# Optimization experiments

Hardware: AMD Instinct MI355X
Metric: run time of the kernel (lower is better)

The kernel has to match this reference:

```python
import jax, jax.numpy as jnp
import numpy as np
from jax import lax

MASK_ID = 0  # sequence_mask pad token

def setup_inputs() -> dict:
    key = jax.random.key(0)
    ks = jax.random.split(key, 7)
    B, T, V, E, U_, O = 256, 128, 10000, 256, 1024, 1024
    return {
        "sequences": jax.random.randint(ks[0], (B, T), 0, V),
        "emb_table": jax.random.normal(ks[1], (V, E), jnp.float32) * 0.02,
        "W": jax.random.normal(ks[2], (E, 4 * U_), jnp.float32) * (1.0 / np.sqrt(E)),
        "U": jax.random.normal(ks[3], (U_, 4 * U_), jnp.float32) * (1.0 / np.sqrt(U_)),
        "b": jnp.zeros((4 * U_,), jnp.float32),
        "fc_W": jax.random.normal(ks[4], (U_, O), jnp.float32) * (1.0 / np.sqrt(U_)),
        "fc_b": jnp.zeros((O,), jnp.float32),
    }

def reference(sequences, emb_table, W, U, b, fc_W, fc_b):
    B, T = sequences.shape
    units = U.shape[0]
    # sequence_length_fn: count of non-pad tokens per row
    lengths = jnp.sum(sequences != MASK_ID, axis=1)  # [B]
    x = emb_table[sequences]                          # [B,T,E]
    # precompute input-to-gate contribution (fuses gate matmuls across time)
    x_gates = jnp.einsum('bte,eg->btg', x, W) + b     # [B,T,4U]
    valid = (jnp.arange(T)[:, None] < lengths[None, :])  # [T,B]

    def step(carry, inp):
        h, c = carry
        xg, v = inp                                   # [B,4U], [B]
        z = xg + h @ U
        i, f, g, o = jnp.split(z, 4, axis=-1)         # keras gate order i,f,c,o
        i = jax.nn.sigmoid(i)
        f = jax.nn.sigmoid(f)
        o = jax.nn.sigmoid(o)
        g = jnp.tanh(g)
        c_new = f * c + i * g
        h_new = o * jnp.tanh(c_new)
        vm = v[:, None]
        # dynamic_rnn: zero output past length, carry state through
        h_out = jnp.where(vm, h_new, 0.0)
        return (jnp.where(vm, h_new, h), jnp.where(vm, c_new, c)), h_out

    init = (jnp.zeros((B, units), x.dtype), jnp.zeros((B, units), x.dtype))
    _, outs = lax.scan(step, init, (jnp.swapaxes(x_gates, 0, 1), valid))
    outputs = jnp.swapaxes(outs, 0, 1)                # [B,T,U]
    return outputs @ fc_W + fc_b                      # [B,T,O]
```

## Files before the change

kernel.cpp:

```cpp
#include <hip/hip_runtime.h>

typedef short bf16x8 __attribute__((ext_vector_type(8)));
typedef float f32x4  __attribute__((ext_vector_type(4)));
typedef int   i32x4  __attribute__((ext_vector_type(4)));

#define DEVINL __device__ __forceinline__

static constexpr size_t SZ_WIM  = 4096ull * 512 * 2;
static constexpr size_t SZ_FCW  = 1024ull * 2048 * 2;
static constexpr size_t SZ_UIM  = 8388608;
static constexpr size_t SZ_EBI  = 10000ull * 512 * 2;
static constexpr size_t SZ_HH   = 33ull * 524288;
static constexpr size_t SZ_CB   = 1048576;
static constexpr size_t SZ_LEN  = 4096;
static constexpr size_t SZ_DIAG = 2048;

DEVINL unsigned short bf16rn(float x){
  unsigned u = __float_as_uint(x);
  unsigned r = (u + 0x7fffu + ((u >> 16) & 1u)) >> 16;
  return (unsigned short)r;
}
DEVINL unsigned short bf16lo(float x){
  unsigned ub = __float_as_uint(x);
  return bf16rn(x - __uint_as_float(ub & 0xffff0000u));
}
DEVINL float sigm(float x){ return 1.f / (1.f + __expf(-x)); }
DEVINL float tanhfast(float x){
  float xc = fminf(15.f, fmaxf(-15.f, x));
  float e = __expf(2.f * xc);
  return (e - 1.f) / (e + 1.f);
}
DEVINL void gl_lds16(const void* g, void* l){
  __builtin_amdgcn_global_load_lds(
      (const __attribute__((address_space(1))) unsigned*)g,
      (__attribute__((address_space(3))) unsigned*)l, 16, 0, 0);
}
DEVINL int hslot(int t){ return t % 33; }

__global__ void __launch_bounds__(256) probe_fill(float* __restrict__ out, int n, float v)
{
  int i = blockIdx.x * 256 + threadIdx.x;
  if (i < n) out[i] = (i == 0) ? v : 0.f;
}

__global__ void __launch_bounds__(64) diag_check(const int* __restrict__ prog,
                                                 float* __restrict__ out)
{
  if (threadIdx.x == 0){
    int miss = 0;
    for (int i = 7; i >= 1; i--) if (prog[i] == 0) miss = i;
    if (miss){
      for (int k = 0; k < 1024; k++) out[k] = 100.0f + (float)miss;
    }
  }
}

__global__ void __launch_bounds__(128) len_kernel(const int* __restrict__ seq,
                                                  int* __restrict__ len,
                                                  int* __restrict__ prog)
{
  int b = blockIdx.x, t = threadIdx.x;
  if (b == 0 && t == 0) prog[1] = 1;
  int pred = (seq[b * 128 + t] != 0) ? 1 : 0;
  unsigned long long m = __ballot(pred);
  __shared__ int cnt[2];
  if ((t & 63) == 0) cnt[t >> 6] = __popcll(m);
  __syncthreads();
  if (t == 0) len[b] = cnt[0] + cnt[1];
}

__global__ void __launch_bounds__(256) prep_split_img(
    const float* __restrict__ S, unsigned short* __restrict__ img, int N, int Ksrc,
    int* __restrict__ prog, int stage)
{
  __shared__ float tile[64][65];
  const int nt = N >> 6;
  const int bn = blockIdx.x % nt, bk = blockIdx.x / nt;
  const int tid = threadIdx.x;
  if (blockIdx.x == 0 && tid == 0) prog[stage] = 1;
  {
    const int kk = tid >> 6, n = tid & 63;
#pragma unroll 4
    for (int i = 0; i < 16; i++){
      int k = i * 4 + kk;
      tile[k][n] = S[(size_t)((bk << 6) + k) * N + (bn << 6) + n];
    }
  }
  __syncthreads();
  {
    const int n4 = tid >> 6, k = tid & 63;
#pragma unroll 4
    for (int i = 0; i < 16; i++){
      int n = i * 4 + n4;
      float v = tile[k][n];
      size_t rowoff = (size_t)((bn << 6) + n) * (2 * Ksrc) + (bk << 6) + k;
      img[rowoff] = (unsigned short)(__float_as_uint(v) >> 16);
      img[rowoff + Ksrc] = bf16lo(v);
    }
  }
}

__global__ void __launch_bounds__(256) prep_emb_img(const float* __restrict__ emb,
                                                    unsigned short* __restrict__ img)
{
  const int v = blockIdx.x, t = threadIdx.x;
  float x = emb[(size_t)v * 256 + t];
  img[(size_t)v * 512 + t]       = (unsigned short)(__float_as_uint(x) >> 16);
  img[(size_t)v * 512 + 256 + t] = bf16lo(x);
}

__global__ void __launch_bounds__(256) prep_uimg(const float* __restrict__ U,
                                                 signed char* __restrict__ img,
                                                 int* __restrict__ prog)
{
  const int bid = blockIdx.x;
  const int nb = bid >> 2, nt4 = bid & 3;
  const int tid = threadIdx.x;
  if (bid == 0 && tid == 0) prog[4] = 1;
  __shared__ signed char lc[16384], ldq[16384];
  const int colbase = nt4 * 1024 + (nb << 4);
  const int kk = tid >> 4, cc = tid & 15;
#pragma unroll 4
  for (int it = 0; it < 64; it++){
    int k = it * 16 + kk;
    float v = U[(size_t)k * 4096 + colbase + cc];
    int q = (int)rintf(v * 131072.f);
    q = q > 32639 ? 32639 : (q < -32639 ? -32639 : q);
    int a = (q + 128) >> 8;
    int d = q - (a << 8);
    lc[(k << 4) + cc]  = (signed char)a;
    ldq[(k << 4) + cc] = (signed char)d;
  }
  __syncthreads();
#pragma unroll
  for (int rep = 0; rep < 4; rep++){
    int idx = rep * 256 + tid;
    int kt = idx >> 6, lane = idx & 63;
    int n = lane & 15, quad = lane >> 4;
    union { signed char b[16]; i32x4 v; } cb_, db_;
#pragma unroll
    for (int j = 0; j < 16; j++){
      int k = (kt << 6) + (quad << 4) + j;
      cb_.b[j] = lc[(k << 4) + n];
      db_.b[j] = ldq[(k << 4) + n];
    }
    size_t base = (size_t)((((nb << 2) + nt4) * 16 + kt) * 2) * 1024;
    *(i32x4*)(img + base + (size_t)lane * 16)        = cb_.v;
    *(i32x4*)(img + base + 1024 + (size_t)lane * 16) = db_.v;
  }
}

__global__ void __launch_bounds__(256) gemm_gates(
    const unsigned short* __restrict__ Aimg, const unsigned short* __restrict__ Bimg,
    const float* __restrict__ bias, unsigned short* __restrict__ D,
    const int* __restrict__ seq, int c0, int tcsh, int* __restrict__ prog)
{
  __shared__ __align__(16) char lds[32768];
  __shared__ int stok[128];
  const int tid = threadIdx.x, lane = tid & 63, wv = tid >> 6;
  const int quad = lane >> 4, nlo = lane & 15;
  const int wm = wv & 1, wn = wv >> 1;
  const int rowbase = (blockIdx.x >> 5) << 7;
  const int colbase = (blockIdx.x & 31) << 7;
  const int tcm1 = (1 << tcsh) - 1;
  if (blockIdx.x == 0 && tid == 0) prog[5] = 1;
  if (tid < 128){
    int r = rowbase + tid;
    stok[tid] = seq[((r >> tcsh) << 7) + c0 + (r & tcm1)];
  }
  __syncthreads();

  f32x4 acc[4][4];
#pragma unroll
  for (int i = 0; i < 4; i++)
#pragma unroll
    for (int j = 0; j < 4; j++) acc[i][j] = (f32x4){0.f, 0.f, 0.f, 0.f};

  const unsigned short* asrc[2]; const unsigned short* bsrc[2];
  char* adst[2]; char* bdst[2];
#pragma unroll
  for (int p = 0; p < 2; p++){
    int gidx = p * 256 + tid;
    int row = gidx >> 2, sg = gidx & 3;
    int sgs = sg ^ ((row >> 1) & 3);
    asrc[p] = Aimg + (size_t)stok[row] * 512 + sgs * 8;
    bsrc[p] = Bimg + (size_t)(colbase + row) * 512 + sgs * 8;
    adst[p] = &lds[p * 4096 + wv * 1024];
    bdst[p] = &lds[16384 + p * 4096 + wv * 1024];
  }

  auto stage = [&](int c, int cur){
    int k0 = c * 32;
    int seg = (k0 >= 512) ? 2 : (k0 >= 256 ? 1 : 0);
    int acol = k0 - seg * 256;
    int aoff = (seg == 1 ? 256 : 0) + acol;
    int boff = (seg == 2 ? 256 : 0) + acol;
#pragma unroll
    for (int p = 0; p < 2; p++){
      gl_lds16(asrc[p] + aoff, adst[p] + cur * 8192);
      gl_lds16(bsrc[p] + boff, bdst[p] + cur * 8192);
    }
  };

  stage(0, 0);
  int cur = 0;
#pragma unroll 2
  for (int c = 0; c < 24; c++){
    __syncthreads();
    if (c + 1 < 24) stage(c + 1, cur ^ 1);
    bf16x8 af[4], bfr[4];
#pragma unroll
    for (int mt = 0; mt < 4; mt++){
      int r = wm * 64 + mt * 16 + nlo;
      af[mt] = *(const bf16x8*)(&lds[cur * 8192 + r * 64 + ((quad ^ ((r >> 1) & 3)) << 4)]);
    }
#pragma unroll
    for (int nt = 0; nt < 4; nt++){
      int r = wn * 64 + nt * 16 + nlo;
      bfr[nt] = *(const bf16x8*)(&lds[16384 + cur * 8192 + r * 64 + ((quad ^ ((r >> 1) & 3)) << 4)]);
    }
#pragma unroll
    for (int mt = 0; mt < 4; mt++)
#pragma unroll
      for (int nt = 0; nt < 4; nt++)
        acc[mt][nt] = __builtin_amdgcn_mfma_f32_16x16x32_bf16(af[mt], bfr[nt], acc[mt][nt], 0, 0, 0);
    cur ^= 1;
  }

  float bs[4];
#pragma unroll
  for (int nt = 0; nt < 4; nt++) bs[nt] = bias[colbase + wn * 64 + nt * 16 + nlo];
#pragma unroll
  for (int mt = 0; mt < 4; mt++)
#pragma unroll
    for (int nt = 0; nt < 4; nt++){
      int col = colbase + wn * 64 + nt * 16 + nlo;
#pragma unroll
      for (int r = 0; r < 4; r++){
        int row = rowbase + wm * 64 + mt * 16 + quad * 4 + r;
        float v = acc[mt][nt][r] + bs[nt];
        int q = (int)rintf(v * 16384.f);
        q = q > 32767 ? 32767 : (q < -32767 ? -32767 : q);
        D[(size_t)row * 4096 + col] = (unsigned short)(short)q;
      }
    }
}

__global__ void __launch_bounds__(256) gemm_out(
    const unsigned short* __restrict__ ohol, const unsigned short* __restrict__ Bimg,
    const float* __restrict__ bias, float* __restrict__ D,
    int c0, int tcsh, int* __restrict__ prog)
{
  __shared__ __align__(16) char lds[32768];
  const int tid = threadIdx.x, lane = tid & 63, wv = tid >> 6;
  const int quad = lane >> 4, nlo = lane & 15;
  const int wm = wv & 1, wn = wv >> 1;
  const int rowbase = (blockIdx.x >> 3) << 7;
  const int colbase = (blockIdx.x & 7) << 7;
  const int tcm1 = (1 << tcsh) - 1;
  if (blockIdx.x == 0 && tid == 0) prog[7] = 1;

  f32x4 acc[4][4];
#pragma unroll
  for (int i = 0; i < 4; i++)
#pragma unroll
    for (int j = 0; j < 4; j++) acc[i][j] = (f32x4){0.f, 0.f, 0.f, 0.f};

  const unsigned short* asrc[2]; const unsigned short* bsrc[2];
  char* adst[2]; char* bdst[2];
#pragma unroll
  for (int p = 0; p < 2; p++){
    int gidx = p * 256 + tid;
    int row = gidx >> 2, sg = gidx & 3;
    int sgs = sg ^ ((row >> 1) & 3);
    asrc[p] = ohol + (size_t)(rowbase + row) * 2048 + sgs * 8;
    bsrc[p] = Bimg + (size_t)(colbase + row) * 2048 + sgs * 8;
    adst[p] = &lds[p * 4096 + wv * 1024];
    bdst[p] = &lds[16384 + p * 4096 + wv * 1024];
  }

  auto stage = [&](int c, int cur){
    int k0 = c * 32;
    int seg = (k0 >= 2048) ? 2 : (k0 >= 1024 ? 1 : 0);
    int acol = k0 - seg * 1024;
    int aoff = (seg == 1 ? 1024 : 0) + acol;
    int boff = (seg == 2 ? 1024 : 0) + acol;
#pragma unroll
    for (int p = 0; p < 2; p++){
      gl_lds16(asrc[p] + aoff, adst[p] + cur * 8192);
      gl_lds16(bsrc[p] + boff, bdst[p] + cur * 8192);
    }
  };

  stage(0, 0);
  int cur = 0;
#pragma unroll 2
  for (int c = 0; c < 96; c++){
    __syncthreads();
    if (c + 1 < 96) stage(c + 1, cur ^ 1);
    bf16x8 af[4], bfr[4];
#pragma unroll
    for (int mt = 0; mt < 4; mt++){
      int r = wm * 64 + mt * 16 + nlo;
      af[mt] = *(const bf16x8*)(&lds[cur * 8192 + r * 64 + ((quad ^ ((r >> 1) & 3)) << 4)]);
    }
#pragma unroll
    for (int nt = 0; nt < 4; nt++){
      int r = wn * 64 + nt * 16 + nlo;
      bfr[nt] = *(const bf16x8*)(&lds[16384 + cur * 8192 + r * 64 + ((quad ^ ((r >> 1) & 3)) << 4)]);
    }
#pragma unroll
    for (int mt = 0; mt < 4; mt++)
#pragma unroll
      for (int nt = 0; nt < 4; nt++)
        acc[mt][nt] = __builtin_amdgcn_mfma_f32_16x16x32_bf16(af[mt], bfr[nt], acc[mt][nt], 0, 0, 0);
    cur ^= 1;
  }

  float bs[4];
#pragma unroll
  for (int nt = 0; nt < 4; nt++) bs[nt] = bias[colbase + wn * 64 + nt * 16 + nlo];
#pragma unroll
  for (int mt = 0; mt < 4; mt++)
#pragma unroll
    for (int nt = 0; nt < 4; nt++){
      int col = colbase + wn * 64 + nt * 16 + nlo;
#pragma unroll
      for (int r = 0; r < 4; r++){
        int row = rowbase + wm * 64 + mt * 16 + quad * 4 + r;
        int drow = ((row >> tcsh) << 7) + c0 + (row & tcm1);
        D[(size_t)drow * 1024 + col] = acc[mt][nt][r] + bs[nt];
      }
    }
}

DEVINL void mbbar(int* flags, int nb, int t, int wv, int lane){
  __syncthreads();
  if (wv == 0){
    if (lane == 0)
      __hip_atomic_store(&flags[nb], t + 1, __ATOMIC_RELAXED, __HIP_MEMORY_SCOPE_AGENT);
    const int tgt = t + 1;
    for (;;){
      int v = __hip_atomic_load(&flags[lane], __ATOMIC_RELAXED, __HIP_MEMORY_SCOPE_AGENT);
      if (__ballot(v >= tgt) == ~0ull) break;
      __builtin_amdgcn_s_sleep(1);
    }
    __builtin_amdgcn_fence(__ATOMIC_ACQUIRE, "workgroup");
  }
  __syncthreads();
}

__global__ void __launch_bounds__(512, 2) lstm_rec(
    const unsigned short* __restrict__ xq,
    const signed char* __restrict__ uimg,
    const int* __restrict__ len,
    signed char* __restrict__ hh,
    float* __restrict__ cbuf,
    unsigned short* __restrict__ ohol,
    int* __restrict__ barbase,
    int* __restrict__ prog,
    int c0, int tcsh)
{
  __shared__ __align__(16) char lds[50176];
  const int tc = 1 << tcsh;
  const int wg = blockIdx.x, mb = wg >> 6, nb = wg & 63;
  const int tid = threadIdx.x, lane = tid & 63, wv = tid >> 6;
  const int quad = lane >> 4, nlo = lane & 15;
  const int mh = wv & 1, g = wv >> 1;
  int* flags = barbase + (mb << 6);
  if (wg == 0 && tid == 0) prog[6] = 1;

  const unsigned short* hh2 = (const unsigned short*)hh;

  i32x4 Bf[16][2];
#pragma unroll
  for (int kt = 0; kt < 16; kt++)
#pragma unroll
    for (int pl = 0; pl < 2; pl++){
      size_t off = (size_t)((((nb << 2) + g) * 16 + kt) * 2 + pl);
      off = (off * 64 + lane) << 4;
      Bf[kt][pl] = *(const i32x4*)(uimg + off);
    }

  const int erow = tid >> 3;
  const int ecp  = tid & 7;
  const int ecol0 = ecp << 1;
  const int ucol0 = (nb << 4) + ecol0;
  const int bglob = (mb << 6) + erow;
  const int lenr = len[bglob];
  float cst[2], hst[2];
#pragma unroll
  for (int r = 0; r < 2; r++){
    cst[r] = cbuf[(size_t)bglob * 1024 + ucol0 + r];
    unsigned short e = hh2[(size_t)hslot(c0) * 262144 + (size_t)bglob * 1024 + ucol0 + r];
    int a = (signed char)(e >> 8), b_ = (signed char)(e & 255);
    hst[r] = (float)(a * 256 + b_) * (1.0f / 32512.0f);
  }

  const int xrow = tid >> 3, xgt = (tid & 7) >> 1, xhf = tid & 1;
  int4 xreg;
  auto load_x = [&](int s){
    size_t grow = (size_t)((((mb << 6) + xrow) << tcsh) + s);
    xreg = *(const int4*)(xq + grow * 4096 + (xgt << 10) + (nb << 4) + (xhf << 3));
  };
  load_x(0);

  const int hrw = tid >> 3, hsub = tid & 7;

#pragma unroll 1
  for (int s = 0; s < tc; s++){
    const int t = c0 + s;
    const signed char* hsrc = hh + (size_t)hslot(t) * 524288 + (size_t)(mb << 6) * 2048;

    i32x4 accH[2], accM[2], accL[2];
#pragma unroll
    for (int m = 0; m < 2; m++){
      accH[m] = (i32x4){0,0,0,0};
      accM[m] = (i32x4){0,0,0,0};
      accL[m] = (i32x4){0,0,0,0};
    }

    int4 hregA[2], hregB[2];
    auto load_hto = [&](int c, int4* dst){
      const signed char* p = hsrc + (size_t)hrw * 2048 + c * 256 + hsub * 32;
      dst[0] = *(const int4*)p;
      dst[1] = *(const int4*)(p + 16);
    };
    auto write_hf = [&](const int4* src){
      unsigned r0 = (unsigned)src[0].x, r1 = (unsigned)src[0].y;
      unsigned r2 = (unsigned)src[0].z, r3 = (unsigned)src[0].w;
      unsigned r4 = (unsigned)src[1].x, r5 = (unsigned)src[1].y;
      unsigned r6 = (unsigned)src[1].z, r7 = (unsigned)src[1].w;
      i32x4 lo, hi;
      lo[0] = __builtin_amdgcn_perm(r1, r0, 0x06040200u);
      lo[1] = __builtin_amdgcn_perm(r3, r2, 0x06040200u);
      lo[2] = __builtin_amdgcn_perm(r5, r4, 0x06040200u);
      lo[3] = __builtin_amdgcn_perm(r7, r6, 0x06040200u);
      hi[0] = __builtin_amdgcn_perm(r1, r0, 0x07050301u);
      hi[1] = __builtin_amdgcn_perm(r3, r2, 0x07050301u);
      hi[2] = __builtin_amdgcn_perm(r5, r4, 0x07050301u);
      hi[3] = __builtin_amdgcn_perm(r7, r6, 0x07050301u);
      int sw = (hsub ^ (hrw & 7)) << 4;
      *(i32x4*)(&lds[hrw * 128 + sw])        = hi;
      *(i32x4*)(&lds[8192 + hrw * 128 + sw]) = lo;
    };

    load_hto(0, hregA);
    load_hto(1, hregB);

#pragma unroll
    for (int c = 0; c < 8; c++){
      __syncthreads();
      if ((c & 1) == 0) write_hf(hregA); else write_hf(hregB);
      if (c == 0){
        union { int4 v; unsigned short u[8]; } xu; xu.v = xreg;
        const float xs = 1.0f / 16384.f;
        float4 f0, f1;
        f0.x = (float)(short)xu.u[0] * xs; f0.y = (float)(short)xu.u[1] * xs;
        f0.z = (float)(short)xu.u[2] * xs; f0.w = (float)(short)xu.u[3] * xs;
        f1.x = (float)(short)xu.u[4] * xs; f1.y = (float)(short)xu.u[5] * xs;
        f1.z = (float)(short)xu.u[6] * xs; f1.w = (float)(short)xu.u[7] * xs;
        char* xb = &lds[16384 + xrow * 256 + (((xgt << 4) + (xhf << 3)) << 2)];
        *(float4*)xb = f0;
        *(float4*)(xb + 16) = f1;
      }
      __syncthreads();
      if (c + 2 < 8){
        if ((c & 1) == 0) load_hto(c + 2, hregA); else load_hto(c + 2, hregB);
      }
#pragma unroll
      for (int kt2 = 0; kt2 < 2; kt2++){
        const int kt = c * 2 + kt2;
        i32x4 Af[2][2];
#pragma unroll
        for (int m = 0; m < 2; m++){
          int hrow = (mh << 5) + (m << 4) + nlo;
          int sgl = ((kt2 << 2) + quad) ^ (hrow & 7);
          Af[m][0] = *(const i32x4*)(&lds[hrow * 128 + (sgl << 4)]);
          Af[m][1] = *(const i32x4*)(&lds[8192 + hrow * 128 + (sgl << 4)]);
        }
#pragma unroll
        for (int m = 0; m < 2; m++){
          accH[m] = __builtin_amdgcn_mfma_i32_16x16x64_i8(Af[m][0], Bf[kt][0], accH[m], 0, 0, 0);
          accM[m] = __builtin_amdgcn_mfma_i32_16x16x64_i8(Af[m][0], Bf[kt][1], accM[m], 0, 0, 0);
          accM[m] = __builtin_amdgcn_mfma_i32_16x16x64_i8(Af[m][1], Bf[kt][0], accM[m], 0, 0, 0);
          accL[m] = __builtin_amdgcn_mfma_i32_16x16x64_i8(Af[m][1], Bf[kt][1], accL[m], 0, 0, 0);
        }
      }
    }
    __syncthreads();

    if (s + 1 < tc) load_x(s + 1);

    const float cH = 1.0f / 65024.0f;
    const float cM = 1.0f / 16646144.0f;
    const float cL = 1.0f / 4261412864.0f;
#pragma unroll
    for (int m = 0; m < 2; m++){
#pragma unroll
      for (int r = 0; r < 4; r++){
        float z = (float)accH[m][r] * cH
                + (float)accM[m][r] * cM
                + (float)accL[m][r] * cL;
        int zrow = (mh << 5) + (m << 4) + (quad << 2) + r;
        *(float*)(&lds[32768 + (((zrow * 68) + g * 16 + nlo) << 2)]) = z;
      }
    }
    __syncthreads();

    {
      float ho16[2];
      unsigned enc2 = 0;
#pragma unroll
      for (int r = 0; r < 2; r++){
        int col = ecol0 + r;
        float zi = *(const float*)(&lds[32768 + (((erow * 68) + 0  + col) << 2)])
                 + *(const float*)(&lds[16384 + (((erow << 6) + 0  + col) << 2)]);
        float zf = *(const float*)(&lds[32768 + (((erow * 68) + 16 + col) << 2)])
                 + *(const float*)(&lds[16384 + (((erow << 6) + 16 + col) << 2)]);
        float zg = *(const float*)(&lds[32768 + (((erow * 68) + 32 + col) << 2)])
                 + *(const float*)(&lds[16384 + (((erow << 6) + 32 + col) << 2)]);
        float zo = *(const float*)(&lds[32768 + (((erow * 68) + 48 + col) << 2)])
                 + *(const float*)(&lds[16384 + (((erow << 6) + 48 + col) << 2)]);
        float iv = sigm(zi), fv = sigm(zf), ov = sigm(zo), gv = tanhfast(zg);
        float cn = fv * cst[r] + iv * gv;
        float hn = ov * tanhfast(cn);
        bool vld = (t < lenr);
        cst[r] = vld ? cn : cst[r];
        hst[r] = vld ? hn : hst[r];
        ho16[r] = vld ? hn : 0.f;
        int H = (int)rintf(hst[r] * 32512.f);
        H = H > 32512 ? 32512 : (H < -32512 ? -32512 : H);
        int a = (H + 128) >> 8;
        int b_ = H - (a << 8);
        unsigned e = (((unsigned)a & 255u) << 8) | ((unsigned)b_ & 255u);
        enc2 |= e << (r * 16);
      }
      size_t orow = ((size_t)bglob << tcsh) + s;
      unsigned hi2 = (unsigned)(__float_as_uint(ho16[0]) >> 16)
                   | ((unsigned)(__float_as_uint(ho16[1]) >> 16) << 16);
      unsigned lo2 = (unsigned)bf16lo(ho16[0]) | ((unsigned)bf16lo(ho16[1]) << 16);
      *(unsigned*)(ohol + orow * 2048 + ucol0)        = hi2;
      *(unsigned*)(ohol + orow * 2048 + 1024 + ucol0) = lo2;
      unsigned* hp = (unsigned*)(hh + (size_t)hslot(t + 1) * 524288
                                 + ((size_t)bglob * 1024 + ucol0) * 2);
      unsigned old = __hip_atomic_exchange(hp, enc2, __ATOMIC_RELAXED,
                                           __HIP_MEMORY_SCOPE_AGENT);
      asm volatile("" :: "v"(old));
    }
    mbbar(flags, nb, t, wv, lane);
  }

#pragma unroll
  for (int r = 0; r < 2; r++)
    cbuf[(size_t)bglob * 1024 + ucol0 + r] = cst[r];
}

extern "C" void kernel_launch(void* const* d_in, const int* in_sizes, int n_in,
                              void* d_out, int out_size, void* d_ws, size_t ws_size,
                              hipStream_t stream)
{
  const int*   seq = (const int*)  d_in[0];
  const float* emb = (const float*)d_in[1];
  const float* Wm  = (const float*)d_in[2];
  const float* Um  = (const float*)d_in[3];
  const float* bv  = (const float*)d_in[4];
  const float* fcW = (const float*)d_in[5];
  const float* fcb = (const float*)d_in[6];
  float* out = (float*)d_out;
  char* ws = (char*)d_ws;

  hipMemsetAsync(d_out, 0x42, 256, stream);

  size_t off = 0;
  unsigned short* wim = (unsigned short*)(ws + off); off += SZ_WIM;
  unsigned short* fcw = (unsigned short*)(ws + off); off += SZ_FCW;
  signed char*    uim = (signed char*)(ws + off);    off += SZ_UIM;
  unsigned short* ebi = (unsigned short*)(ws + off); off += SZ_EBI;
  signed char*    hh  = (signed char*)(ws + off);    off += SZ_HH;
  float*          cb  = (float*)(ws + off);          off += SZ_CB;
  int*            len = (int*)(ws + off);            off += SZ_LEN;
  int*            diag= (int*)(ws + off);            off += SZ_DIAG;
  const size_t fixed = off;

  int tcsh = -1;
  for (int s = 5; s >= 0; s--)
    if (ws && fixed + (3145728ull << s) <= ws_size){ tcsh = s; break; }

  if (tcsh < 0){
    probe_fill<<<(out_size + 255) / 256, 256, 0, stream>>>(
        out, out_size, 1000.0f + (float)(ws_size >> 20));
    return;
  }
  const int tc = 1 << tcsh;

  unsigned short* xqc  = (unsigned short*)(ws + fixed);
  unsigned short* ohol = (unsigned short*)(ws + fixed + (size_t)tc * 2097152);

  hipMemsetAsync(diag, 0, SZ_DIAG, stream);
  hipMemsetAsync(hh, 0, 524288, stream);
  hipMemsetAsync(cb, 0, SZ_CB, stream);

  int* prog = diag;
  int* barbase = diag + 64;

  len_kernel<<<256, 128, 0, stream>>>(seq, len, prog);
  prep_split_img<<<256, 256, 0, stream>>>(Wm, wim, 4096, 256, prog, 2);
  prep_split_img<<<256, 256, 0, stream>>>(fcW, fcw, 1024, 1024, prog, 3);
  prep_emb_img<<<10000, 256, 0, stream>>>(emb, ebi);
  prep_uimg<<<256, 256, 0, stream>>>(Um, uim, prog);

  for (int c0 = 0; c0 < 128; c0 += tc){
    gemm_gates<<<dim3((2 * tc) * 32), 256, 0, stream>>>(ebi, wim, bv, xqc, seq, c0, tcsh, prog);
    lstm_rec<<<dim3(256), 512, 0, stream>>>(xqc, uim, len, hh, cb, ohol, barbase, prog, c0, tcsh);
    gemm_out<<<dim3((2 * tc) * 8), 256, 0, stream>>>(ohol, fcw, fcb, out, c0, tcsh, prog);
  }

  diag_check<<<1, 64, 0, stream>>>(prog, out);
}
```

Before: 1.880 ms.

## Split recurrent LSTM batch tile across twice as many workgroups

The persistent recurrent kernel now launches 512 workgroups, each handling 32 batch rows instead of 64. Per-workgroup LDS, MFMA work and h staging are halved, and only half the threads run the elementwise gate update. The intent is to spread the serial per-timestep work over more CUs and shorten each step's critical path. In exchange there are twice as many barrier participants and flag groups, the launch bound asks for higher occupancy, and the B-fragment registers from U are duplicated across more blocks.

```diff
diff --git a/kernel.cpp b/kernel.cpp
--- a/kernel.cpp
+++ b/kernel.cpp
@@ -13,7 +13,7 @@
 static constexpr size_t SZ_HH   = 33ull * 524288;
 static constexpr size_t SZ_CB   = 1048576;
 static constexpr size_t SZ_LEN  = 4096;
-static constexpr size_t SZ_DIAG = 2048;
+static constexpr size_t SZ_DIAG = 4096;
 
 DEVINL unsigned short bf16rn(float x){
   unsigned u = __float_as_uint(x);
@@ -350,7 +350,7 @@
   __syncthreads();
 }
 
-__global__ void __launch_bounds__(512, 2) lstm_rec(
+__global__ void __launch_bounds__(512, 4) lstm_rec(
     const unsigned short* __restrict__ xq,
     const signed char* __restrict__ uimg,
     const int* __restrict__ len,
@@ -361,7 +361,7 @@
     int* __restrict__ prog,
     int c0, int tcsh)
 {
-  __shared__ __align__(16) char lds[50176];
+  __shared__ __align__(16) char lds[25088];
   const int tc = 1 << tcsh;
   const int wg = blockIdx.x, mb = wg >> 6, nb = wg & 63;
   const int tid = threadIdx.x, lane = tid & 63, wv = tid >> 6;
@@ -382,110 +382,91 @@
       Bf[kt][pl] = *(const i32x4*)(uimg + off);
     }
 
-  const int erow = tid >> 3;
-  const int ecp  = tid & 7;
-  const int ecol0 = ecp << 1;
-  const int ucol0 = (nb << 4) + ecol0;
-  const int bglob = (mb << 6) + erow;
-  const int lenr = len[bglob];
-  float cst[2], hst[2];
-#pragma unroll
-  for (int r = 0; r < 2; r++){
-    cst[r] = cbuf[(size_t)bglob * 1024 + ucol0 + r];
-    unsigned short e = hh2[(size_t)hslot(c0) * 262144 + (size_t)bglob * 1024 + ucol0 + r];
-    int a = (signed char)(e >> 8), b_ = (signed char)(e & 255);
-    hst[r] = (float)(a * 256 + b_) * (1.0f / 32512.0f);
-  }
-
-  const int xrow = tid >> 3, xgt = (tid & 7) >> 1, xhf = tid & 1;
-  int4 xreg;
+  const bool ew = (tid < 256);
+  int erow = 0, ecol0 = 0, ucol0 = 0, bglob = 0, lenr = 0;
+  float cst[2] = {0.f, 0.f}, hst[2] = {0.f, 0.f};
+  if (ew){
+    erow  = tid >> 3;
+    ecol0 = (tid & 7) << 1;
+    ucol0 = (nb << 4) + ecol0;
+    bglob = (mb << 5) + erow;
+    lenr  = len[bglob];
+#pragma unroll
+    for (int r = 0; r < 2; r++){
+      cst[r] = cbuf[(size_t)bglob * 1024 + ucol0 + r];
+      unsigned short e = hh2[(size_t)hslot(c0) * 262144 + (size_t)bglob * 1024 + ucol0 + r];
+      int a = (signed char)(e >> 8), b_ = (signed char)(e & 255);
+      hst[r] = (float)(a * 256 + b_) * (1.0f / 32512.0f);
+    }
+  }
+
+  const int xrow = tid >> 4, xgt = (tid >> 2) & 3, xq4 = tid & 3;
+  int2 xreg;
   auto load_x = [&](int s){
-    size_t grow = (size_t)((((mb << 6) + xrow) << tcsh) + s);
-    xreg = *(const int4*)(xq + grow * 4096 + (xgt << 10) + (nb << 4) + (xhf << 3));
+    size_t grow = (size_t)((((mb << 5) + xrow) << tcsh) + s);
+    xreg = *(const int2*)(xq + grow * 4096 + (xgt << 10) + (nb << 4) + (xq4 << 2));
   };
   load_x(0);
 
-  const int hrw = tid >> 3, hsub = tid & 7;
+  const int hrw = tid >> 4, hsub = tid & 15;
 
 #pragma unroll 1
   for (int s = 0; s < tc; s++){
     const int t = c0 + s;
-    const signed char* hsrc = hh + (size_t)hslot(t) * 524288 + (size_t)(mb << 6) * 2048;
-
-    i32x4 accH[2], accM[2], accL[2];
-#pragma unroll
-    for (int m = 0; m < 2; m++){
-      accH[m] = (i32x4){0,0,0,0};
-      accM[m] = (i32x4){0,0,0,0};
-      accL[m] = (i32x4){0,0,0,0};
-    }
-
-    int4 hregA[2], hregB[2];
+    const signed char* hsrc = hh + (size_t)hslot(t) * 524288 + (size_t)(mb << 5) * 2048;
+
+    i32x4 accH = (i32x4){0,0,0,0};
+    i32x4 accM = (i32x4){0,0,0,0};
+    i32x4 accL = (i32x4){0,0,0,0};
+
+    int4 hregA, hregB;
     auto load_hto = [&](int c, int4* dst){
-      const signed char* p = hsrc + (size_t)hrw * 2048 + c * 256 + hsub * 32;
-      dst[0] = *(const int4*)p;
-      dst[1] = *(const int4*)(p + 16);
+      *dst = *(const int4*)(hsrc + (size_t)hrw * 2048 + c * 256 + hsub * 16);
     };
     auto write_hf = [&](const int4* src){
-      unsigned r0 = (unsigned)src[0].x, r1 = (unsigned)src[0].y;
-      unsigned r2 = (unsigned)src[0].z, r3 = (unsigned)src[0].w;
-      unsigned r4 = (unsigned)src[1].x, r5 = (unsigned)src[1].y;
-      unsigned r6 = (unsigned)src[1].z, r7 = (unsigned)src[1].w;
-      i32x4 lo, hi;
-      lo[0] = __builtin_amdgcn_perm(r1, r0, 0x06040200u);
-      lo[1] = __builtin_amdgcn_perm(r3, r2, 0x06040200u);
-      lo[2] = __builtin_amdgcn_perm(r5, r4, 0x06040200u);
-      lo[3] = __builtin_amdgcn_perm(r7, r6, 0x06040200u);
-      hi[0] = __builtin_amdgcn_perm(r1, r0, 0x07050301u);
-      hi[1] = __builtin_amdgcn_perm(r3, r2, 0x07050301u);
-      hi[2] = __builtin_amdgcn_perm(r5, r4, 0x07050301u);
-      hi[3] = __builtin_amdgcn_perm(r7, r6, 0x07050301u);
-      int sw = (hsub ^ (hrw & 7)) << 4;
-      *(i32x4*)(&lds[hrw * 128 + sw])        = hi;
-      *(i32x4*)(&lds[8192 + hrw * 128 + sw]) = lo;
+      unsigned w0 = (unsigned)src->x, w1 = (unsigned)src->y;
+      unsigned w2 = (unsigned)src->z, w3 = (unsigned)src->w;
+      int2 lo, hi;
+      lo.x = (int)__builtin_amdgcn_perm(w1, w0, 0x06040200u);
+      lo.y = (int)__builtin_amdgcn_perm(w3, w2, 0x06040200u);
+      hi.x = (int)__builtin_amdgcn_perm(w1, w0, 0x07050301u);
+      hi.y = (int)__builtin_amdgcn_perm(w3, w2, 0x07050301u);
+      int sg = (hsub >> 1) ^ (hrw & 7);
+      int off = hrw * 128 + (sg << 4) + ((hsub & 1) << 3);
+      *(int2*)(&lds[off])        = hi;
+      *(int2*)(&lds[4096 + off]) = lo;
     };
 
-    load_hto(0, hregA);
-    load_hto(1, hregB);
+    load_hto(0, &hregA);
+    load_hto(1, &hregB);
 
 #pragma unroll
     for (int c = 0; c < 8; c++){
       __syncthreads();
-      if ((c & 1) == 0) write_hf(hregA); else write_hf(hregB);
+      if ((c & 1) == 0) write_hf(&hregA); else write_hf(&hregB);
       if (c == 0){
-        union { int4 v; unsigned short u[8]; } xu; xu.v = xreg;
+        union { int2 v; unsigned short u[4]; } xu; xu.v = xreg;
         const float xs = 1.0f / 16384.f;
-        float4 f0, f1;
+        float4 f0;
         f0.x = (float)(short)xu.u[0] * xs; f0.y = (float)(short)xu.u[1] * xs;
         f0.z = (float)(short)xu.u[2] * xs; f0.w = (float)(short)xu.u[3] * xs;
-        f1.x = (float)(short)xu.u[4] * xs; f1.y = (float)(short)xu.u[5] * xs;
-        f1.z = (float)(short)xu.u[6] * xs; f1.w = (float)(short)xu.u[7] * xs;
-        char* xb = &lds[16384 + xrow * 256 + (((xgt << 4) + (xhf << 3)) << 2)];
-        *(float4*)xb = f0;
-        *(float4*)(xb + 16) = f1;
+        *(float4*)(&lds[8192 + xrow * 256 + (((xgt << 4) + (xq4 << 2)) << 2)]) = f0;
       }
       __syncthreads();
       if (c + 2 < 8){
-        if ((c & 1) == 0) load_hto(c + 2, hregA); else load_hto(c + 2, hregB);
+        if ((c & 1) == 0) load_hto(c + 2, &hregA); else load_hto(c + 2, &hregB);
       }
 #pragma unroll
       for (int kt2 = 0; kt2 < 2; kt2++){
         const int kt = c * 2 + kt2;
-        i32x4 Af[2][2];
-#pragma unroll
-        for (int m = 0; m < 2; m++){
-          int hrow = (mh << 5) + (m << 4) + nlo;
-          int sgl = ((kt2 << 2) + quad) ^ (hrow & 7);
-          Af[m][0] = *(const i32x4*)(&lds[hrow * 128 + (sgl << 4)]);
-          Af[m][1] = *(const i32x4*)(&lds[8192 + hrow * 128 + (sgl << 4)]);
-        }
-#pragma unroll
-        for (int m = 0; m < 2; m++){
-          accH[m] = __builtin_amdgcn_mfma_i32_16x16x64_i8(Af[m][0], Bf[kt][0], accH[m], 0, 0, 0);
-          accM[m] = __builtin_amdgcn_mfma_i32_16x16x64_i8(Af[m][0], Bf[kt][1], accM[m], 0, 0, 0);
-          accM[m] = __builtin_amdgcn_mfma_i32_16x16x64_i8(Af[m][1], Bf[kt][0], accM[m], 0, 0, 0);
-          accL[m] = __builtin_amdgcn_mfma_i32_16x16x64_i8(Af[m][1], Bf[kt][1], accL[m], 0, 0, 0);
-        }
+        const int hrow = (mh << 4) + nlo;
+        const int sgl = ((kt2 << 2) + quad) ^ (hrow & 7);
+        i32x4 Af0 = *(const i32x4*)(&lds[hrow * 128 + (sgl << 4)]);
+        i32x4 Af1 = *(const i32x4*)(&lds[4096 + hrow * 128 + (sgl << 4)]);
+        accH = __builtin_amdgcn_mfma_i32_16x16x64_i8(Af0, Bf[kt][0], accH, 0, 0, 0);
+        accM = __builtin_amdgcn_mfma_i32_16x16x64_i8(Af0, Bf[kt][1], accM, 0, 0, 0);
+        accM = __builtin_amdgcn_mfma_i32_16x16x64_i8(Af1, Bf[kt][0], accM, 0, 0, 0);
+        accL = __builtin_amdgcn_mfma_i32_16x16x64_i8(Af1, Bf[kt][1], accL, 0, 0, 0);
       }
     }
     __syncthreads();
@@ -496,32 +477,29 @@
     const float cM = 1.0f / 16646144.0f;
     const float cL = 1.0f / 4261412864.0f;
 #pragma unroll
-    for (int m = 0; m < 2; m++){
-#pragma unroll
-      for (int r = 0; r < 4; r++){
-        float z = (float)accH[m][r] * cH
-                + (float)accM[m][r] * cM
-                + (float)accL[m][r] * cL;
-        int zrow = (mh << 5) + (m << 4) + (quad << 2) + r;
-        *(float*)(&lds[32768 + (((zrow * 68) + g * 16 + nlo) << 2)]) = z;
-      }
+    for (int r = 0; r < 4; r++){
+      float z = (float)accH[r] * cH
+              + (float)accM[r] * cM
+              + (float)accL[r] * cL;
+      int zrow = (mh << 4) + (quad << 2) + r;
+      *(float*)(&lds[16384 + (((zrow * 68) + g * 16 + nlo) << 2)]) = z;
     }
     __syncthreads();
 
-    {
+    if (ew){
       float ho16[2];
       unsigned enc2 = 0;
 #pragma unroll
       for (int r = 0; r < 2; r++){
         int col = ecol0 + r;
-        float zi = *(const float*)(&lds[32768 + (((erow * 68) + 0  + col) << 2)])
-                 + *(const float*)(&lds[16384 + (((erow << 6) + 0  + col) << 2)]);
-        float zf = *(const float*)(&lds[32768 + (((erow * 68) + 16 + col) << 2)])
-                 + *(const float*)(&lds[16384 + (((erow << 6) + 16 + col) << 2)]);
-        float zg = *(const float*)(&lds[32768 + (((erow * 68) + 32 + col) << 2)])
-                 + *(const float*)(&lds[16384 + (((erow << 6) + 32 + col) << 2)]);
-        float zo = *(const float*)(&lds[32768 + (((erow * 68) + 48 + col) << 2)])
-                 + *(const float*)(&lds[16384 + (((erow << 6) + 48 + col) << 2)]);
+        float zi = *(const float*)(&lds[16384 + (((erow * 68) + 0  + col) << 2)])
+                 + *(const float*)(&lds[8192  + (((erow << 6) + 0  + col) << 2)]);
+        float zf = *(const float*)(&lds[16384 + (((erow * 68) + 16 + col) << 2)])
+                 + *(const float*)(&lds[8192  + (((erow << 6) + 16 + col) << 2)]);
+        float zg = *(const float*)(&lds[16384 + (((erow * 68) + 32 + col) << 2)])
+                 + *(const float*)(&lds[8192  + (((erow << 6) + 32 + col) << 2)]);
+        float zo = *(const float*)(&lds[16384 + (((erow * 68) + 48 + col) << 2)])
+                 + *(const float*)(&lds[8192  + (((erow << 6) + 48 + col) << 2)]);
         float iv = sigm(zi), fv = sigm(zf), ov = sigm(zo), gv = tanhfast(zg);
         float cn = fv * cst[r] + iv * gv;
         float hn = ov * tanhfast(cn);
@@ -551,9 +529,11 @@
     mbbar(flags, nb, t, wv, lane);
   }
 
-#pragma unroll
-  for (int r = 0; r < 2; r++)
-    cbuf[(size_t)bglob * 1024 + ucol0 + r] = cst[r];
+  if (ew){
+#pragma unroll
+    for (int r = 0; r < 2; r++)
+      cbuf[(size_t)bglob * 1024 + ucol0 + r] = cst[r];
+  }
 }
 
 extern "C" void kernel_launch(void* const* d_in, const int* in_sizes, int n_in,
@@ -612,7 +592,7 @@
 
   for (int c0 = 0; c0 < 128; c0 += tc){
     gemm_gates<<<dim3((2 * tc) * 32), 256, 0, stream>>>(ebi, wim, bv, xqc, seq, c0, tcsh, prog);
-    lstm_rec<<<dim3(256), 512, 0, stream>>>(xqc, uim, len, hh, cb, ohol, barbase, prog, c0, tcsh);
+    lstm_rec<<<dim3(512), 512, 0, stream>>>(xqc, uim, len, hh, cb, ohol, barbase, prog, c0, tcsh);
     gemm_out<<<dim3((2 * tc) * 8), 256, 0, stream>>>(ohol, fcw, fcb, out, c0, tcsh, prog);
   }
 
```

Result: slower. 3.515 ms (+87.0%).
